# Kernel tuning notes

Measured on AMD Instinct MI355X. Metric: run time of the kernel, lower is better.

The kernel has to match this reference:

```python
import jax, jax.numpy as jnp
import numpy as np

B, S, DIM, H, HD = 2, 2048, 512, 8, 64
VD = DIM // H  # 64
QK = H * HD


def setup_inputs() -> dict:
    key = jax.random.key(0)
    k1, k2, k3, k4, k5 = jax.random.split(key, 5)
    x = jax.random.normal(k1, (B, S, DIM), dtype=jnp.float32)
    mask = jax.random.bernoulli(k2, 0.5, (B, S))
    # per-position rotation matrices, scaled to keep activations O(1)
    rotator = jax.random.normal(k3, (B, S, HD, HD), dtype=jnp.float32) / np.sqrt(HD)
    # torch Linear weights: [out_features, in_features], no bias
    W_trans = jax.random.normal(k4, (2 * QK + DIM, DIM), dtype=jnp.float32) / np.sqrt(DIM)
    W_o = jax.random.normal(k5, (DIM, DIM), dtype=jnp.float32) / np.sqrt(DIM)
    return {"x": x, "mask": mask, "rotator": rotator, "W_trans": W_trans, "W_o": W_o}


def _taylor_attention(qs, ks, vs, mask):
    # 2nd-order Taylor approximation of exp for softmax weights
    # qs/ks: [B,S,H,HD], vs: [B,S,H,VD], mask: [B,S] key mask
    scores = jnp.einsum('bqhd,bkhd->bhqk', qs, ks) / np.sqrt(HD)
    w = 1.0 + scores + 0.5 * scores * scores
    w = jnp.where(mask[:, None, None, :], w, 0.0)
    w = w / jnp.sum(w, axis=-1, keepdims=True)
    out = jnp.einsum('bhqk,bkhd->bqhd', w, vs)
    return out.reshape(out.shape[0], out.shape[1], -1)  # [B,S,DIM]


def reference(x, mask, rotator, W_trans, W_o):
    t = x @ W_trans.T  # [B,S,2*QK+DIM]
    qs = t[..., :QK].reshape(B, S, H, HD)
    ks = t[..., QK:2 * QK].reshape(B, S, H, HD)
    vs = t[..., 2 * QK:].reshape(B, S, H, VD)
    sel = mask[..., None, None]
    qs = jnp.where(sel, jnp.einsum('bsij,bshj->bshi', rotator, qs), qs)
    ks = jnp.where(sel, jnp.einsum('bsij,bshj->bshi', rotator, ks), ks)
    out = _taylor_attention(qs, ks, vs, mask)
    return out @ W_o.T
```

## Files before the change

kernel.cpp:

```cpp
#include <hip/hip_runtime.h>
#include <hip/hip_bf16.h>

#define B_    2
#define S_    2048
#define DIM_  512
#define H_    8
#define HD_   64
#define TOUT_ 1536
#define ROWS_ (B_ * S_)

typedef unsigned short ushort_t;
typedef __attribute__((ext_vector_type(8))) __bf16 bf16x8;
typedef __attribute__((ext_vector_type(4))) float floatx4;

#define AS_GLB __attribute__((address_space(1)))
#define AS_LDS __attribute__((address_space(3)))

__device__ __forceinline__ float bf2f(unsigned int u) { return __uint_as_float(u << 16); }
__device__ __forceinline__ unsigned short f2bfu(float f) {
    unsigned u = __float_as_uint(f);
    unsigned r = (u + 0x7fffu + ((u >> 16) & 1u)) >> 16;
    return (unsigned short)r;
}
__device__ __forceinline__ bf16x8 cvt8(const float* p) {
    float4 a = *reinterpret_cast<const float4*>(p);
    float4 b = *reinterpret_cast<const float4*>(p + 4);
    ushort_t o[8] = {f2bfu(a.x), f2bfu(a.y), f2bfu(a.z), f2bfu(a.w),
                     f2bfu(b.x), f2bfu(b.y), f2bfu(b.z), f2bfu(b.w)};
    return *reinterpret_cast<bf16x8*>(o);
}

__global__ void tmha_detect(const unsigned char* mb, int* flags) {
    __shared__ int s_bf, s_f, s_u8;
    int tid = threadIdx.x;
    if (tid == 0) { s_bf = 0; s_f = 0; s_u8 = 0; }
    __syncthreads();
    int cbf = 0, cf = 0, cu8 = 0;
    for (int i = tid; i < 4096; i += 256) {
        unsigned char v = mb[i];
        if (v == 0x3F || v == 0x80) {
            cf++;
            if ((i & 3) == 1) cbf++;
        } else if (v != 0 && (i & 3) != 0) {
            cu8++;
        }
    }
    atomicAdd(&s_bf, cbf); atomicAdd(&s_f, cf); atomicAdd(&s_u8, cu8);
    __syncthreads();
    if (tid == 0) {
        int mcls;
        if (s_bf > 0)      mcls = 2;
        else if (s_f > 0)  mcls = 3;
        else if (s_u8 > 0) mcls = 0;
        else               mcls = 1;
        flags[1] = mcls;
    }
}

__global__ void tmha_decode_mask(const unsigned char* mb, const int* flags, int* wm) {
    int i = blockIdx.x * 256 + threadIdx.x;
    if (i >= ROWS_) return;
    int cls = flags[1];
    int v;
    if (cls == 0)      v = (mb[i] != 0);
    else if (cls == 1) v = (reinterpret_cast<const int*>(mb)[i] != 0);
    else if (cls == 2) v = ((reinterpret_cast<const unsigned short*>(mb)[i] & 0x7fffu) != 0);
    else               v = ((reinterpret_cast<const unsigned int*>(mb)[i] & 0x7fffffffu) != 0);
    wm[i] = v;
}

__global__ __launch_bounds__(256) void cast_bf16(const float* __restrict__ src,
                                                 ushort_t* __restrict__ dst, int n4) {
    int i = blockIdx.x * 256 + threadIdx.x;
    if (i >= n4) return;
    float4 v = reinterpret_cast<const float4*>(src)[i];
    ushort_t o[4] = {f2bfu(v.x), f2bfu(v.y), f2bfu(v.z), f2bfu(v.w)};
    reinterpret_cast<uint2*>(dst)[i] = *reinterpret_cast<uint2*>(o);
}

template <int TM, int N, int K>
__global__ __launch_bounds__(256) void mfma_gemm_bt(const ushort_t* __restrict__ A,
                                                    const ushort_t* __restrict__ Bm,
                                                    float* __restrict__ C) {
    constexpr int FM = TM / 32;
    __shared__ __align__(16) ushort_t As[TM * 64];
    __shared__ __align__(16) ushort_t Bs[128 * 64];
    int tid = threadIdx.x;
    int lane = tid & 63;
    int wv = tid >> 6;
    int wm = wv >> 1, wn = wv & 1;
    int quad = lane >> 4;
    int mrow = lane & 15;
    int bx = blockIdx.x;
    int by = blockIdx.y;

    floatx4 acc[FM][4];
#pragma unroll
    for (int i = 0; i < FM; i++)
#pragma unroll
        for (int j = 0; j < 4; j++) acc[i][j] = (floatx4){0.f, 0.f, 0.f, 0.f};

    for (int k0 = 0; k0 < K; k0 += 64) {
#pragma unroll
        for (int t = 0; t < TM / 32; t++) {
            int p = (wv * (TM / 32) + t) * 64 + lane;
            int row = p >> 3, cp = p & 7;
            int gc = cp ^ (row & 7);
            const ushort_t* ga = A + (size_t)(by * TM + row) * K + k0 + gc * 8;
            __builtin_amdgcn_global_load_lds((const AS_GLB unsigned int*)ga,
                                             (AS_LDS unsigned int*)&As[(size_t)(wv * (TM / 32) + t) * 64 * 8],
                                             16, 0, 0);
        }
#pragma unroll
        for (int t = 0; t < 4; t++) {
            int p = (wv * 4 + t) * 64 + lane;
            int row = p >> 3, cp = p & 7;
            int gc = cp ^ (row & 7);
            const ushort_t* gb = Bm + (size_t)(bx * 128 + row) * K + k0 + gc * 8;
            __builtin_amdgcn_global_load_lds((const AS_GLB unsigned int*)gb,
                                             (AS_LDS unsigned int*)&Bs[(size_t)(wv * 4 + t) * 64 * 8],
                                             16, 0, 0);
        }
        __syncthreads();
#pragma unroll
        for (int ks = 0; ks < 64; ks += 32) {
            int c = (ks >> 3) + quad;
            bf16x8 af[FM], bf[4];
#pragma unroll
            for (int i = 0; i < FM; i++) {
                int row = wm * (TM / 2) + i * 16 + mrow;
                int pos = row * 8 + (c ^ (row & 7));
                af[i] = *reinterpret_cast<const bf16x8*>(&As[pos * 8]);
            }
#pragma unroll
            for (int j = 0; j < 4; j++) {
                int row = wn * 64 + j * 16 + mrow;
                int pos = row * 8 + (c ^ (row & 7));
                bf[j] = *reinterpret_cast<const bf16x8*>(&Bs[pos * 8]);
            }
#pragma unroll
            for (int i = 0; i < FM; i++)
#pragma unroll
                for (int j = 0; j < 4; j++)
                    acc[i][j] = __builtin_amdgcn_mfma_f32_16x16x32_bf16(af[i], bf[j], acc[i][j], 0, 0, 0);
        }
        __syncthreads();
    }

    int col0 = bx * 128 + wn * 64 + mrow;
    int row0 = by * TM + wm * (TM / 2) + quad * 4;
#pragma unroll
    for (int i = 0; i < FM; i++)
#pragma unroll
        for (int j = 0; j < 4; j++)
#pragma unroll
            for (int r = 0; r < 4; r++)
                C[(size_t)(row0 + i * 16 + r) * N + col0 + j * 16] = acc[i][j][r];
}

__global__ __launch_bounds__(256) void rot_qk_mfma(const float* __restrict__ t,
                                                   const float* __restrict__ rotG,
                                                   const int* __restrict__ wm,
                                                   ushort_t* __restrict__ Qb,
                                                   ushort_t* __restrict__ Kb) {
    int lane = threadIdx.x & 63;
    int wv = threadIdx.x >> 6;
    int row = blockIdx.x * 4 + wv;
    int b = row >> 11, s = row & 2047;
    int lm = lane & 15, quad = lane >> 4;
    const float* trow = t + (size_t)row * TOUT_;

    if (wm[row]) {
        bf16x8 af[2];
#pragma unroll
        for (int kc = 0; kc < 2; kc++)
            af[kc] = cvt8(trow + lm * 64 + kc * 32 + quad * 8);

        const float* R = rotG + (size_t)row * 4096;
        floatx4 dacc[4];
#pragma unroll
        for (int nb = 0; nb < 4; nb++) dacc[nb] = (floatx4){0.f, 0.f, 0.f, 0.f};
#pragma unroll
        for (int nb = 0; nb < 4; nb++)
#pragma unroll
            for (int kc = 0; kc < 2; kc++) {
                bf16x8 bfr = cvt8(R + (size_t)(nb * 16 + lm) * 64 + kc * 32 + quad * 8);
                dacc[nb] = __builtin_amdgcn_mfma_f32_16x16x32_bf16(af[kc], bfr, dacc[nb], 0, 0, 0);
            }
#pragma unroll
        for (int nb = 0; nb < 4; nb++)
#pragma unroll
            for (int r = 0; r < 4; r++) {
                int vec = quad * 4 + r;
                int h = vec & 7;
                ushort_t* dst = (vec >= 8 ? Kb : Qb);
                dst[((size_t)(b * 8 + h) * 2048 + s) * 64 + nb * 16 + lm] = f2bfu(dacc[nb][r]);
            }
    } else {
#pragma unroll
        for (int nb = 0; nb < 4; nb++)
#pragma unroll
            for (int r = 0; r < 4; r++) {
                int vec = quad * 4 + r;
                int h = vec & 7;
                float v = trow[vec * 64 + nb * 16 + lm];
                ushort_t* dst = (vec >= 8 ? Kb : Qb);
                dst[((size_t)(b * 8 + h) * 2048 + s) * 64 + nb * 16 + lm] = f2bfu(v);
            }
    }
}

__global__ __launch_bounds__(256) void prep_vt(const float* __restrict__ t,
                                               const int* __restrict__ wm,
                                               ushort_t* __restrict__ VtG) {
    __shared__ float tile[64][65];
    __shared__ float mrow[64];
    int st = blockIdx.x;
    int bh = blockIdx.y;
    int b = bh >> 3, h = bh & 7;
    int tid = threadIdx.x;
    if (tid < 64) mrow[tid] = wm[b * 2048 + st * 64 + tid] ? 1.0f : 0.0f;
#pragma unroll
    for (int i = 0; i < 4; i++) {
        int q = i * 256 + tid;
        int r = q >> 4, c4 = (q & 15) * 4;
        float4 v = *reinterpret_cast<const float4*>(
            t + (size_t)(b * 2048 + st * 64 + r) * TOUT_ + 1024 + h * 64 + c4);
        tile[r][c4] = v.x; tile[r][c4 + 1] = v.y; tile[r][c4 + 2] = v.z; tile[r][c4 + 3] = v.w;
    }
    __syncthreads();
#pragma unroll
    for (int i = 0; i < 8; i++) {
        int e = i * 256 + tid;
        int d = e >> 5, sl = (e & 31) * 2;
        float v0 = tile[sl][d] * mrow[sl];
        float v1 = tile[sl + 1][d] * mrow[sl + 1];
        unsigned int u = (unsigned)f2bfu(v0) | ((unsigned)f2bfu(v1) << 16);
        *reinterpret_cast<unsigned int*>(VtG + ((size_t)bh * 65 + d) * 2048 + st * 64 + sl) = u;
    }
    if (tid < 32) {
        int sl = tid * 2;
        unsigned m0 = mrow[sl]     != 0.f ? 0x3F80u : 0u;
        unsigned m1 = mrow[sl + 1] != 0.f ? 0x3F80u : 0u;
        *reinterpret_cast<unsigned int*>(VtG + ((size_t)bh * 65 + 64) * 2048 + st * 64 + sl) = m0 | (m1 << 16);
    }
}

__global__ __launch_bounds__(256) void tmha_attn_mfma(const ushort_t* __restrict__ Qb,
                                                      const ushort_t* __restrict__ Kb,
                                                      const ushort_t* __restrict__ VtG,
                                                      float* __restrict__ numer,
                                                      float* __restrict__ den) {
    __shared__ __align__(16) ushort_t Ks[1024 * 8];
    __shared__ __align__(16) ushort_t Vs[1280 * 8];
    __shared__ __align__(16) ushort_t Ps[1024 * 8];
    int tid = threadIdx.x;
    int lane = tid & 63;
    int wv = tid >> 6;
    int lm = lane & 15;
    int quad = lane >> 4;
    int qt = blockIdx.x;
    int h = blockIdx.y;
    int z = blockIdx.z;
    int b = z >> 1;
    int ks = z & 1;
    int bh = b * 8 + h;

    for (int i = tid; i < 960; i += 256)
        reinterpret_cast<unsigned int*>(&Vs[1040 * 8])[i] = 0u;

    bf16x8 qf[2];
    {
        const ushort_t* qp = Qb + ((size_t)bh * 2048 + qt * 64 + wv * 16 + lm) * 64 + quad * 8;
        qf[0] = *reinterpret_cast<const bf16x8*>(qp);
        qf[1] = *reinterpret_cast<const bf16x8*>(qp + 32);
    }

    floatx4 oacc[5];
#pragma unroll
    for (int j = 0; j < 5; j++) oacc[j] = (floatx4){0.f, 0.f, 0.f, 0.f};

    for (int kt = ks * 1024; kt < ks * 1024 + 1024; kt += 128) {
#pragma unroll
        for (int t4 = 0; t4 < 4; t4++) {
            int p = (wv * 4 + t4) * 64 + lane;
            int row = p >> 3, cp = p & 7;
            int gc = cp ^ (row & 7);
            const ushort_t* g = Kb + ((size_t)bh * 2048 + kt + row) * 64 + gc * 8;
            __builtin_amdgcn_global_load_lds((const AS_GLB unsigned int*)g,
                                             (AS_LDS unsigned int*)&Ks[(size_t)(wv * 4 + t4) * 64 * 8],
                                             16, 0, 0);
        }
#pragma unroll
        for (int t4 = 0; t4 < 4; t4++) {
            int p = (wv * 4 + t4) * 64 + lane;
            int row = p >> 4, cp = p & 15;
            int gc = cp ^ (row & 15);
            const ushort_t* g = VtG + ((size_t)bh * 65 + row) * 2048 + kt + gc * 8;
            __builtin_amdgcn_global_load_lds((const AS_GLB unsigned int*)g,
                                             (AS_LDS unsigned int*)&Vs[(size_t)(wv * 4 + t4) * 64 * 8],
                                             16, 0, 0);
        }
        if (tid < 64) {
            unsigned int mv = *reinterpret_cast<const unsigned int*>(
                VtG + ((size_t)bh * 65 + 64) * 2048 + kt + tid * 2);
            reinterpret_cast<unsigned int*>(&Vs[1024 * 8])[tid] = mv;
        }
        __syncthreads();

        floatx4 sacc[8];
#pragma unroll
        for (int j = 0; j < 8; j++) sacc[j] = (floatx4){0.f, 0.f, 0.f, 0.f};
#pragma unroll
        for (int j = 0; j < 8; j++) {
            int row = j * 16 + lm;
#pragma unroll
            for (int kc = 0; kc < 2; kc++) {
                int c = kc * 4 + quad;
                int pos = row * 8 + (c ^ (row & 7));
                bf16x8 bk = *reinterpret_cast<const bf16x8*>(&Ks[pos * 8]);
                sacc[j] = __builtin_amdgcn_mfma_f32_16x16x32_bf16(qf[kc], bk, sacc[j], 0, 0, 0);
            }
        }

#pragma unroll
        for (int j = 0; j < 8; j++)
#pragma unroll
            for (int r = 0; r < 4; r++) {
                float s = sacc[j][r];
                float wgt = fmaf(s, fmaf(s, 0.0078125f, 0.125f), 1.0f);
                int m = wv * 16 + quad * 4 + r;
                int col = j * 16 + lm;
                int cw = col >> 3;
                int pos = m * 16 + (cw ^ (m & 15));
                Ps[pos * 8 + (col & 7)] = f2bfu(wgt);
            }
        __syncthreads();

#pragma unroll
        for (int j = 0; j < 5; j++) {
            int vrow = j * 16 + lm;
#pragma unroll
            for (int kc = 0; kc < 4; kc++) {
                int c = kc * 4 + quad;
                int ppos = (wv * 16 + lm) * 16 + (c ^ lm);
                bf16x8 pa = *reinterpret_cast<const bf16x8*>(&Ps[ppos * 8]);
                int vpos = vrow * 16 + (c ^ (vrow & 15));
                bf16x8 vb = *reinterpret_cast<const bf16x8*>(&Vs[vpos * 8]);
                oacc[j] = __builtin_amdgcn_mfma_f32_16x16x32_bf16(pa, vb, oacc[j], 0, 0, 0);
            }
        }
        __syncthreads();
    }

#pragma unroll
    for (int j = 0; j < 4; j++)
#pragma unroll
        for (int r = 0; r < 4; r++) {
            int qrow = b * 2048 + qt * 64 + wv * 16 + quad * 4 + r;
            numer[((size_t)ks * ROWS_ + qrow) * DIM_ + h * 64 + j * 16 + lm] = oacc[j][r];
        }
    if (lm == 0) {
#pragma unroll
        for (int r = 0; r < 4; r++) {
            int qrow = b * 2048 + qt * 64 + wv * 16 + quad * 4 + r;
            den[((size_t)ks * ROWS_ + qrow) * 8 + h] = oacc[4][r];
        }
    }
}

__global__ __launch_bounds__(256) void attn_combine(const float* __restrict__ numer,
                                                    const float* __restrict__ den,
                                                    ushort_t* __restrict__ attnAb) {
    int i = blockIdx.x * 256 + threadIdx.x;
    int row = i >> 7;
    int c4 = (i & 127) * 4;
    int h = c4 >> 6;
    float4 n0 = *reinterpret_cast<const float4*>(&numer[(size_t)row * DIM_ + c4]);
    float4 n1 = *reinterpret_cast<const float4*>(&numer[((size_t)ROWS_ + row) * DIM_ + c4]);
    float d = den[(size_t)row * 8 + h] + den[((size_t)ROWS_ + row) * 8 + h];
    float inv = 1.0f / d;
    ushort_t o[4] = {f2bfu((n0.x + n1.x) * inv), f2bfu((n0.y + n1.y) * inv),
                     f2bfu((n0.z + n1.z) * inv), f2bfu((n0.w + n1.w) * inv)};
    *reinterpret_cast<uint2*>(&attnAb[(size_t)row * DIM_ + c4]) = *reinterpret_cast<uint2*>(o);
}

extern "C" void kernel_launch(void* const* d_in, const int* in_sizes, int n_in,
                              void* d_out, int out_size, void* d_ws, size_t ws_size,
                              hipStream_t stream) {
    (void)in_sizes; (void)n_in; (void)out_size; (void)ws_size;
    const float* x    = (const float*)d_in[0];
    const void*  mask = d_in[1];
    const float* rot  = (const float*)d_in[2];
    const float* Wt   = (const float*)d_in[3];
    const float* Wo   = (const float*)d_in[4];

    char* ws = (char*)d_ws;
    int* flags       = (int*)ws;
    int* wmask       = (int*)(ws + 64);
    float* t         = (float*)(ws + 32768);
    ushort_t* Xb     = (ushort_t*)(ws + 25198592);
    ushort_t* Wtb    = (ushort_t*)(ws + 29392896);
    ushort_t* Wob    = (ushort_t*)(ws + 30965760);
    ushort_t* Qb     = (ushort_t*)(ws + 31490048);
    ushort_t* Kb     = (ushort_t*)(ws + 35684352);
    ushort_t* VtG    = (ushort_t*)(ws + 39878656);
    ushort_t* attnAb = (ushort_t*)(ws + 44138496);
    float* numer     = t;
    float* den       = (float*)(ws + 32768 + 16777216);

    tmha_detect<<<1, 256, 0, stream>>>((const unsigned char*)mask, flags);
    tmha_decode_mask<<<16, 256, 0, stream>>>((const unsigned char*)mask, flags, wmask);

    cast_bf16<<<(ROWS_ * DIM_ / 4 + 255) / 256, 256, 0, stream>>>(x, Xb, ROWS_ * DIM_ / 4);
    cast_bf16<<<(TOUT_ * DIM_ / 4 + 255) / 256, 256, 0, stream>>>(Wt, Wtb, TOUT_ * DIM_ / 4);
    cast_bf16<<<(DIM_ * DIM_ / 4 + 255) / 256, 256, 0, stream>>>(Wo, Wob, DIM_ * DIM_ / 4);

    {
        dim3 grid(TOUT_ / 128, ROWS_ / 64);
        mfma_gemm_bt<64, TOUT_, DIM_><<<grid, 256, 0, stream>>>(Xb, Wtb, t);
    }

    rot_qk_mfma<<<ROWS_ / 4, 256, 0, stream>>>(t, rot, wmask, Qb, Kb);

    {
        dim3 grid(32, 16);
        prep_vt<<<grid, 256, 0, stream>>>(t, wmask, VtG);
    }

    {
        dim3 grid(32, 8, 4);
        tmha_attn_mfma<<<grid, 256, 0, stream>>>(Qb, Kb, VtG, numer, den);
    }
    attn_combine<<<(ROWS_ * 128) / 256, 256, 0, stream>>>(numer, den, attnAb);

    {
        dim3 grid(DIM_ / 128, ROWS_ / 64);
        mfma_gemm_bt<64, DIM_, DIM_><<<grid, 256, 0, stream>>>(attnAb, Wob, (float*)d_out);
    }
}
```

Before: 204.3 us.

## Store projection output in bf16 and shrink attention key tile

The QKV projection GEMM now writes its output in bf16 instead of fp32. The rotation and V-transpose kernels read those bf16 values directly, which halves the intermediate write and read traffic. The attention kernel moves from 128-key to 64-key tiles with smaller LDS buffers, loads the mask row via global_load_lds, and replaces the intra-iteration barrier with a wave-local lgkmcnt wait, since each wave only reads its own P rows. This adds more loop iterations and zeroes the denominator operand per lane, and the fp32 intermediate now carries extra bf16 rounding before the rotation.

```diff
diff --git a/kernel.cpp b/kernel.cpp
--- a/kernel.cpp
+++ b/kernel.cpp
@@ -78,10 +78,10 @@
     reinterpret_cast<uint2*>(dst)[i] = *reinterpret_cast<uint2*>(o);
 }
 
-template <int TM, int N, int K>
+template <int TM, int N, int K, bool OUT_BF16>
 __global__ __launch_bounds__(256) void mfma_gemm_bt(const ushort_t* __restrict__ A,
                                                     const ushort_t* __restrict__ Bm,
-                                                    float* __restrict__ C) {
+                                                    void* __restrict__ Cout) {
     constexpr int FM = TM / 32;
     __shared__ __align__(16) ushort_t As[TM * 64];
     __shared__ __align__(16) ushort_t Bs[128 * 64];
@@ -149,16 +149,28 @@
 
     int col0 = bx * 128 + wn * 64 + mrow;
     int row0 = by * TM + wm * (TM / 2) + quad * 4;
-#pragma unroll
-    for (int i = 0; i < FM; i++)
-#pragma unroll
-        for (int j = 0; j < 4; j++)
-#pragma unroll
-            for (int r = 0; r < 4; r++)
-                C[(size_t)(row0 + i * 16 + r) * N + col0 + j * 16] = acc[i][j][r];
-}
-
-__global__ __launch_bounds__(256) void rot_qk_mfma(const float* __restrict__ t,
+    if constexpr (OUT_BF16) {
+        ushort_t* C = reinterpret_cast<ushort_t*>(Cout);
+#pragma unroll
+        for (int i = 0; i < FM; i++)
+#pragma unroll
+            for (int j = 0; j < 4; j++)
+#pragma unroll
+                for (int r = 0; r < 4; r++)
+                    C[(size_t)(row0 + i * 16 + r) * N + col0 + j * 16] = f2bfu(acc[i][j][r]);
+    } else {
+        float* C = reinterpret_cast<float*>(Cout);
+#pragma unroll
+        for (int i = 0; i < FM; i++)
+#pragma unroll
+            for (int j = 0; j < 4; j++)
+#pragma unroll
+                for (int r = 0; r < 4; r++)
+                    C[(size_t)(row0 + i * 16 + r) * N + col0 + j * 16] = acc[i][j][r];
+    }
+}
+
+__global__ __launch_bounds__(256) void rot_qk_mfma(const ushort_t* __restrict__ t,
                                                    const float* __restrict__ rotG,
                                                    const int* __restrict__ wm,
                                                    ushort_t* __restrict__ Qb,
@@ -168,13 +180,13 @@
     int row = blockIdx.x * 4 + wv;
     int b = row >> 11, s = row & 2047;
     int lm = lane & 15, quad = lane >> 4;
-    const float* trow = t + (size_t)row * TOUT_;
+    const ushort_t* trow = t + (size_t)row * TOUT_;
 
     if (wm[row]) {
         bf16x8 af[2];
 #pragma unroll
         for (int kc = 0; kc < 2; kc++)
-            af[kc] = cvt8(trow + lm * 64 + kc * 32 + quad * 8);
+            af[kc] = *reinterpret_cast<const bf16x8*>(trow + lm * 64 + kc * 32 + quad * 8);
 
         const float* R = rotG + (size_t)row * 4096;
         floatx4 dacc[4];
@@ -203,17 +215,16 @@
             for (int r = 0; r < 4; r++) {
                 int vec = quad * 4 + r;
                 int h = vec & 7;
-                float v = trow[vec * 64 + nb * 16 + lm];
                 ushort_t* dst = (vec >= 8 ? Kb : Qb);
-                dst[((size_t)(b * 8 + h) * 2048 + s) * 64 + nb * 16 + lm] = f2bfu(v);
-            }
-    }
-}
-
-__global__ __launch_bounds__(256) void prep_vt(const float* __restrict__ t,
+                dst[((size_t)(b * 8 + h) * 2048 + s) * 64 + nb * 16 + lm] = trow[vec * 64 + nb * 16 + lm];
+            }
+    }
+}
+
+__global__ __launch_bounds__(256) void prep_vt(const ushort_t* __restrict__ t,
                                                const int* __restrict__ wm,
                                                ushort_t* __restrict__ VtG) {
-    __shared__ float tile[64][65];
+    __shared__ ushort_t tile[64][72];
     __shared__ float mrow[64];
     int st = blockIdx.x;
     int bh = blockIdx.y;
@@ -221,22 +232,21 @@
     int tid = threadIdx.x;
     if (tid < 64) mrow[tid] = wm[b * 2048 + st * 64 + tid] ? 1.0f : 0.0f;
 #pragma unroll
-    for (int i = 0; i < 4; i++) {
+    for (int i = 0; i < 2; i++) {
         int q = i * 256 + tid;
-        int r = q >> 4, c4 = (q & 15) * 4;
-        float4 v = *reinterpret_cast<const float4*>(
-            t + (size_t)(b * 2048 + st * 64 + r) * TOUT_ + 1024 + h * 64 + c4);
-        tile[r][c4] = v.x; tile[r][c4 + 1] = v.y; tile[r][c4 + 2] = v.z; tile[r][c4 + 3] = v.w;
+        int r = q >> 3, c8 = (q & 7) * 8;
+        uint4 v = *reinterpret_cast<const uint4*>(
+            t + (size_t)(b * 2048 + st * 64 + r) * TOUT_ + 1024 + h * 64 + c8);
+        *reinterpret_cast<uint4*>(&tile[r][c8]) = v;
     }
     __syncthreads();
 #pragma unroll
     for (int i = 0; i < 8; i++) {
         int e = i * 256 + tid;
         int d = e >> 5, sl = (e & 31) * 2;
-        float v0 = tile[sl][d] * mrow[sl];
-        float v1 = tile[sl + 1][d] * mrow[sl + 1];
-        unsigned int u = (unsigned)f2bfu(v0) | ((unsigned)f2bfu(v1) << 16);
-        *reinterpret_cast<unsigned int*>(VtG + ((size_t)bh * 65 + d) * 2048 + st * 64 + sl) = u;
+        unsigned u0 = (mrow[sl]     != 0.f) ? (unsigned)tile[sl][d]     : 0u;
+        unsigned u1 = (mrow[sl + 1] != 0.f) ? (unsigned)tile[sl + 1][d] : 0u;
+        *reinterpret_cast<unsigned int*>(VtG + ((size_t)bh * 65 + d) * 2048 + st * 64 + sl) = u0 | (u1 << 16);
     }
     if (tid < 32) {
         int sl = tid * 2;
@@ -251,9 +261,9 @@
                                                       const ushort_t* __restrict__ VtG,
                                                       float* __restrict__ numer,
                                                       float* __restrict__ den) {
-    __shared__ __align__(16) ushort_t Ks[1024 * 8];
-    __shared__ __align__(16) ushort_t Vs[1280 * 8];
-    __shared__ __align__(16) ushort_t Ps[1024 * 8];
+    __shared__ __align__(16) ushort_t Ks[512 * 8];
+    __shared__ __align__(16) ushort_t Vs[520 * 8];
+    __shared__ __align__(16) ushort_t Ps[512 * 8];
     int tid = threadIdx.x;
     int lane = tid & 63;
     int wv = tid >> 6;
@@ -266,9 +276,6 @@
     int ks = z & 1;
     int bh = b * 8 + h;
 
-    for (int i = tid; i < 960; i += 256)
-        reinterpret_cast<unsigned int*>(&Vs[1040 * 8])[i] = 0u;
-
     bf16x8 qf[2];
     {
         const ushort_t* qp = Qb + ((size_t)bh * 2048 + qt * 64 + wv * 16 + lm) * 64 + quad * 8;
@@ -276,43 +283,47 @@
         qf[1] = *reinterpret_cast<const bf16x8*>(qp + 32);
     }
 
+    bf16x8 vzero;
+    *reinterpret_cast<uint4*>(&vzero) = (uint4){0u, 0u, 0u, 0u};
+
     floatx4 oacc[5];
 #pragma unroll
     for (int j = 0; j < 5; j++) oacc[j] = (floatx4){0.f, 0.f, 0.f, 0.f};
 
-    for (int kt = ks * 1024; kt < ks * 1024 + 1024; kt += 128) {
-#pragma unroll
-        for (int t4 = 0; t4 < 4; t4++) {
-            int p = (wv * 4 + t4) * 64 + lane;
+    for (int kt = ks * 1024; kt < ks * 1024 + 1024; kt += 64) {
+#pragma unroll
+        for (int t4 = 0; t4 < 2; t4++) {
+            int p = (wv * 2 + t4) * 64 + lane;
             int row = p >> 3, cp = p & 7;
             int gc = cp ^ (row & 7);
             const ushort_t* g = Kb + ((size_t)bh * 2048 + kt + row) * 64 + gc * 8;
             __builtin_amdgcn_global_load_lds((const AS_GLB unsigned int*)g,
-                                             (AS_LDS unsigned int*)&Ks[(size_t)(wv * 4 + t4) * 64 * 8],
+                                             (AS_LDS unsigned int*)&Ks[(size_t)(wv * 2 + t4) * 64 * 8],
                                              16, 0, 0);
         }
 #pragma unroll
-        for (int t4 = 0; t4 < 4; t4++) {
-            int p = (wv * 4 + t4) * 64 + lane;
-            int row = p >> 4, cp = p & 15;
-            int gc = cp ^ (row & 15);
+        for (int t4 = 0; t4 < 2; t4++) {
+            int p = (wv * 2 + t4) * 64 + lane;
+            int row = p >> 3, cp = p & 7;
+            int gc = cp ^ (row & 7);
             const ushort_t* g = VtG + ((size_t)bh * 65 + row) * 2048 + kt + gc * 8;
             __builtin_amdgcn_global_load_lds((const AS_GLB unsigned int*)g,
-                                             (AS_LDS unsigned int*)&Vs[(size_t)(wv * 4 + t4) * 64 * 8],
+                                             (AS_LDS unsigned int*)&Vs[(size_t)(wv * 2 + t4) * 64 * 8],
                                              16, 0, 0);
         }
-        if (tid < 64) {
-            unsigned int mv = *reinterpret_cast<const unsigned int*>(
-                VtG + ((size_t)bh * 65 + 64) * 2048 + kt + tid * 2);
-            reinterpret_cast<unsigned int*>(&Vs[1024 * 8])[tid] = mv;
+        if (tid < 8) {
+            const ushort_t* g = VtG + ((size_t)bh * 65 + 64) * 2048 + kt + tid * 8;
+            __builtin_amdgcn_global_load_lds((const AS_GLB unsigned int*)g,
+                                             (AS_LDS unsigned int*)&Vs[512 * 8],
+                                             16, 0, 0);
         }
         __syncthreads();
 
-        floatx4 sacc[8];
-#pragma unroll
-        for (int j = 0; j < 8; j++) sacc[j] = (floatx4){0.f, 0.f, 0.f, 0.f};
-#pragma unroll
-        for (int j = 0; j < 8; j++) {
+        floatx4 sacc[4];
+#pragma unroll
+        for (int j = 0; j < 4; j++) sacc[j] = (floatx4){0.f, 0.f, 0.f, 0.f};
+#pragma unroll
+        for (int j = 0; j < 4; j++) {
             int row = j * 16 + lm;
 #pragma unroll
             for (int kc = 0; kc < 2; kc++) {
@@ -324,7 +335,7 @@
         }
 
 #pragma unroll
-        for (int j = 0; j < 8; j++)
+        for (int j = 0; j < 4; j++)
 #pragma unroll
             for (int r = 0; r < 4; r++) {
                 float s = sacc[j][r];
@@ -332,21 +343,23 @@
                 int m = wv * 16 + quad * 4 + r;
                 int col = j * 16 + lm;
                 int cw = col >> 3;
-                int pos = m * 16 + (cw ^ (m & 15));
+                int pos = m * 8 + (cw ^ (m & 7));
                 Ps[pos * 8 + (col & 7)] = f2bfu(wgt);
             }
-        __syncthreads();
-
+        asm volatile("s_waitcnt lgkmcnt(0)" ::: "memory");
+
+        int qrow_l = wv * 16 + lm;
 #pragma unroll
         for (int j = 0; j < 5; j++) {
-            int vrow = j * 16 + lm;
-#pragma unroll
-            for (int kc = 0; kc < 4; kc++) {
+            int vrow = (j < 4) ? (j * 16 + lm) : 64;
+#pragma unroll
+            for (int kc = 0; kc < 2; kc++) {
                 int c = kc * 4 + quad;
-                int ppos = (wv * 16 + lm) * 16 + (c ^ lm);
+                int ppos = qrow_l * 8 + (c ^ (qrow_l & 7));
                 bf16x8 pa = *reinterpret_cast<const bf16x8*>(&Ps[ppos * 8]);
-                int vpos = vrow * 16 + (c ^ (vrow & 15));
+                int vpos = vrow * 8 + (c ^ (vrow & 7));
                 bf16x8 vb = *reinterpret_cast<const bf16x8*>(&Vs[vpos * 8]);
+                if (j == 4 && lm != 0) vb = vzero;
                 oacc[j] = __builtin_amdgcn_mfma_f32_16x16x32_bf16(pa, vb, oacc[j], 0, 0, 0);
             }
         }
@@ -398,7 +411,7 @@
     char* ws = (char*)d_ws;
     int* flags       = (int*)ws;
     int* wmask       = (int*)(ws + 64);
-    float* t         = (float*)(ws + 32768);
+    ushort_t* t      = (ushort_t*)(ws + 32768);
     ushort_t* Xb     = (ushort_t*)(ws + 25198592);
     ushort_t* Wtb    = (ushort_t*)(ws + 29392896);
     ushort_t* Wob    = (ushort_t*)(ws + 30965760);
@@ -406,7 +419,7 @@
     ushort_t* Kb     = (ushort_t*)(ws + 35684352);
     ushort_t* VtG    = (ushort_t*)(ws + 39878656);
     ushort_t* attnAb = (ushort_t*)(ws + 44138496);
-    float* numer     = t;
+    float* numer     = (float*)(ws + 32768);
     float* den       = (float*)(ws + 32768 + 16777216);
 
     tmha_detect<<<1, 256, 0, stream>>>((const unsigned char*)mask, flags);
@@ -418,7 +431,7 @@
 
     {
         dim3 grid(TOUT_ / 128, ROWS_ / 64);
-        mfma_gemm_bt<64, TOUT_, DIM_><<<grid, 256, 0, stream>>>(Xb, Wtb, t);
+        mfma_gemm_bt<64, TOUT_, DIM_, true><<<grid, 256, 0, stream>>>(Xb, Wtb, (void*)t);
     }
 
     rot_qk_mfma<<<ROWS_ / 4, 256, 0, stream>>>(t, rot, wmask, Qb, Kb);
@@ -436,6 +449,6 @@
 
     {
         dim3 grid(DIM_ / 128, ROWS_ / 64);
-        mfma_gemm_bt<64, DIM_, DIM_><<<grid, 256, 0, stream>>>(attnAb, Wob, (float*)d_out);
-    }
-}
+        mfma_gemm_bt<64, DIM_, DIM_, false><<<grid, 256, 0, stream>>>(attnAb, Wob, d_out);
+    }
+}
```

Measured after the change: 194.7 us. 1.05x faster.
